# Performance work log

Measured on AMD Instinct MI355X. Metric: run time of the kernel, lower is better.

Reference implementation:

```python
import jax, jax.numpy as jnp
import numpy as np
from jax import lax

K = 4
H = 1024
IN = 512
OUT = 8192
T = 128
B = 32


def setup_inputs() -> dict:
    key = jax.random.key(0)
    ks = jax.random.split(key, 5)
    return {
        "X": jax.random.normal(ks[0], (T, B, IN), dtype=jnp.float32),
        "Wxh_w": jax.random.normal(ks[1], (H, IN), dtype=jnp.float32) * 0.02,
        "Wxh_b": jax.random.normal(ks[2], (H,), dtype=jnp.float32) * 0.02,
        "Whh_w": jax.random.normal(ks[3], (H, (K - 1) * H), dtype=jnp.float32) * 0.02,
        "Wmo_w": jax.random.normal(ks[4], (OUT, K * H), dtype=jnp.float32) * 0.02,
    }


def reference(X, Wxh_w, Wxh_b, Whh_w, Wmo_w):
    batch = X.shape[1]
    # history stack hs: [K-1, B, H], hs[0] = oldest, hs[-1] = newest
    hs0 = jnp.zeros((K - 1, batch, H), dtype=X.dtype)

    def step(hs, x_t):
        # concat reversed(h_prevs): newest block first -> [B, (K-1)*H]
        h_cat = hs[::-1].transpose(1, 0, 2).reshape(batch, (K - 1) * H)
        h_t = jax.nn.selu(x_t @ Wxh_w.T + Wxh_b + h_cat @ Whh_w.T)  # [B, H]
        h_out = jnp.concatenate([h_t, h_cat], axis=1)  # [B, K*H]
        out_t = h_out @ Wmo_w.T  # [B, OUT]
        new_hs = jnp.concatenate([hs[1:], h_t[None]], axis=0)
        # truncated BPTT: detach the (new) oldest hidden
        new_hs = new_hs.at[0].set(lax.stop_gradient(new_hs[0]))
        return new_hs, out_t

    _, outs = lax.scan(step, hs0, X)
    return outs  # [T, B, OUT]
```

## Files before the change

kernel.cpp:

```cpp
#include <hip/hip_runtime.h>
#include <hip/hip_bf16.h>

#define T_STEPS 128
#define BATCH   32
#define IN_DIM  512
#define H_DIM   1024
#define OUT_DIM 8192
#define KH      3072
#define NWG     128
#define SLOT_E  32768
#define NSLOT   131

typedef __attribute__((ext_vector_type(8))) short short8;
typedef __attribute__((ext_vector_type(4))) float f32x4;

__device__ __forceinline__ unsigned short bf16_rne(float f) {
  unsigned u = __float_as_uint(f);
  unsigned r = (u + 0x7FFFu + ((u >> 16) & 1u)) >> 16;
  return (unsigned short)r;
}

__device__ __forceinline__ void gload_lds16(const void* g, void* l) {
  __builtin_amdgcn_global_load_lds(
      (const __attribute__((address_space(1))) void*)g,
      (__attribute__((address_space(3))) void*)l, 16, 0, 0);
}

__global__ __launch_bounds__(256) void convert_kernel(
    const float* __restrict__ src, unsigned short* __restrict__ dst, int n4) {
  int i = blockIdx.x * blockDim.x + threadIdx.x;
  const int stride = gridDim.x * blockDim.x;
  for (; i < n4; i += stride) {
    float4 v = ((const float4*)src)[i];
    ushort4 o;
    o.x = bf16_rne(v.x); o.y = bf16_rne(v.y);
    o.z = bf16_rne(v.z); o.w = bf16_rne(v.w);
    ((ushort4*)dst)[i] = o;
  }
}

__global__ __launch_bounds__(256) void pre_kernel(
    const float* __restrict__ X, const float* __restrict__ Wxh,
    const float* __restrict__ bias, float* __restrict__ preT) {
  __shared__ float xs[32][260];
  const int tid = threadIdx.x;
  const int t  = blockIdx.x >> 4;
  const int jb = blockIdx.x & 15;
  const int b  = tid & 31;
  const int jg = tid >> 5;
  float acc[8];
  #pragma unroll
  for (int i = 0; i < 8; ++i) acc[i] = 0.f;

  for (int kc = 0; kc < 2; ++kc) {
    __syncthreads();
    #pragma unroll
    for (int v = tid; v < 2048; v += 256) {
      int br = v >> 6, i4 = v & 63;
      float4 x4 = *(const float4*)(X + (size_t)t*(BATCH*IN_DIM) + (size_t)br*IN_DIM + kc*256 + i4*4);
      *(float4*)&xs[br][i4*4] = x4;
    }
    __syncthreads();
    for (int i = 0; i < 256; i += 4) {
      const int k = kc*256 + i;
      float4 xv = *(const float4*)&xs[b][i];
      #pragma unroll
      for (int jj = 0; jj < 8; ++jj) {
        const int j = jb*64 + jg + jj*8;
        float4 w4 = *(const float4*)(Wxh + (size_t)j*IN_DIM + k);
        acc[jj] += xv.x*w4.x + xv.y*w4.y + xv.z*w4.z + xv.w*w4.w;
      }
    }
  }
  #pragma unroll
  for (int jj = 0; jj < 8; ++jj) {
    const int j = jb*64 + jg + jj*8;
    preT[(size_t)t*(H_DIM*BATCH) + (size_t)j*BATCH + b] = acc[jj] + bias[j];
  }
}

template<int RN, int RD1, int RD2>
__device__ __forceinline__ void do_step(
    const int t, const int tid, const int wg, const int j0,
    const int lane, const int wv,
    const short8* __restrict__ wf, const short8* __restrict__ hi8,
    const short8* __restrict__ lo8, const float* __restrict__ preT,
    unsigned short* __restrict__ hHi, unsigned short* __restrict__ hLo,
    int* __restrict__ grp, int* __restrict__ rootcnt, int* __restrict__ rootrep,
    short8 (&Rh0)[3][4], short8 (&Rh1)[3][4],
    short8 (&Rl0)[3][4], short8 (&Rl1)[3][4],
    float (&red)[8][16][33],
    unsigned short (&hpk_hi)[32][8], unsigned short (&hpk_lo)[32][8]) {
  f32x4 a0h = {}, a0l = {}, a1h = {}, a1l = {};

  #pragma unroll
  for (int i = 0; i < 4; ++i) {
    const int ks = 32 + wv*4 + i;
    const short8 af = wf[ks*64 + lane];
    a0h = __builtin_amdgcn_mfma_f32_16x16x32_bf16(af, Rh0[RD1][i], a0h, 0, 0, 0);
    a1h = __builtin_amdgcn_mfma_f32_16x16x32_bf16(af, Rh1[RD1][i], a1h, 0, 0, 0);
    a0l = __builtin_amdgcn_mfma_f32_16x16x32_bf16(af, Rl0[RD1][i], a0l, 0, 0, 0);
    a1l = __builtin_amdgcn_mfma_f32_16x16x32_bf16(af, Rl1[RD1][i], a1l, 0, 0, 0);
  }
  #pragma unroll
  for (int i = 0; i < 4; ++i) {
    const int ks = 64 + wv*4 + i;
    const short8 af = wf[ks*64 + lane];
    a0h = __builtin_amdgcn_mfma_f32_16x16x32_bf16(af, Rh0[RD2][i], a0h, 0, 0, 0);
    a1h = __builtin_amdgcn_mfma_f32_16x16x32_bf16(af, Rh1[RD2][i], a1h, 0, 0, 0);
    a0l = __builtin_amdgcn_mfma_f32_16x16x32_bf16(af, Rl0[RD2][i], a0l, 0, 0, 0);
    a1l = __builtin_amdgcn_mfma_f32_16x16x32_bf16(af, Rl1[RD2][i], a1l, 0, 0, 0);
  }

  float upre = 0.f;
  if (tid < 256)
    upre = preT[(size_t)t*(H_DIM*BATCH) + (size_t)(j0 + (tid >> 5))*BATCH + (tid & 31)];

  if (t > 0) {
    if (tid == 0) {
      while (!__hip_atomic_load(&rootrep[(((t-1) << 3) + (wg & 7)) << 4],
                                __ATOMIC_RELAXED, __HIP_MEMORY_SCOPE_AGENT))
        __builtin_amdgcn_s_sleep(2);
    }
    __syncthreads();
    asm volatile("" ::: "memory");
  }

  {
    const size_t sb = (size_t)(128 - t) * 4096;
    #pragma unroll
    for (int i = 0; i < 4; ++i) {
      const int ks = wv*4 + i;
      const size_t bidx = sb + (size_t)ks*128 + (size_t)(lane >> 4)*32 + (lane & 15);
      Rh0[RN][i] = hi8[bidx];
      Rh1[RN][i] = hi8[bidx + 16];
      Rl0[RN][i] = lo8[bidx];
      Rl1[RN][i] = lo8[bidx + 16];
    }
  }
  #pragma unroll
  for (int i = 0; i < 4; ++i) {
    const int ks = wv*4 + i;
    const short8 af = wf[ks*64 + lane];
    a0h = __builtin_amdgcn_mfma_f32_16x16x32_bf16(af, Rh0[RN][i], a0h, 0, 0, 0);
    a1h = __builtin_amdgcn_mfma_f32_16x16x32_bf16(af, Rh1[RN][i], a1h, 0, 0, 0);
    a0l = __builtin_amdgcn_mfma_f32_16x16x32_bf16(af, Rl0[RN][i], a0l, 0, 0, 0);
    a1l = __builtin_amdgcn_mfma_f32_16x16x32_bf16(af, Rl1[RN][i], a1l, 0, 0, 0);
  }

  const f32x4 s0 = a0h + a0l;
  const f32x4 s1 = a1h + a1l;
  const int rr = (lane >> 4) * 4, cc = lane & 15;
  #pragma unroll
  for (int q = 0; q < 4; ++q) {
    red[wv][rr + q][cc]      = s0[q];
    red[wv][rr + q][16 + cc] = s1[q];
  }
  __syncthreads();

  if (tid < 256) {
    const int jj = tid >> 5, b = tid & 31;
    float u = upre;
    #pragma unroll
    for (int w = 0; w < 8; ++w)
      u += red[w][jj][b] + red[w][jj + 8][b];
    const float h = u > 0.f ? 1.0507009873554805f*u
                            : (1.0507009873554805f*1.6732632423543772f)*expm1f(u);
    const unsigned short hh = bf16_rne(h);
    hpk_hi[b][jj] = hh;
    hpk_lo[b][jj] = bf16_rne(h - __uint_as_float((unsigned)hh << 16));
  }
  __syncthreads();

  if (tid < 32) {
    const int b = tid;
    const size_t base = (size_t)(127 - t)*SLOT_E + (size_t)(j0 >> 3)*256 + (size_t)b*8;
    const unsigned long long h0 = *(const unsigned long long*)&hpk_hi[b][0];
    const unsigned long long h1 = *(const unsigned long long*)&hpk_hi[b][4];
    const unsigned long long l0 = *(const unsigned long long*)&hpk_lo[b][0];
    const unsigned long long l1 = *(const unsigned long long*)&hpk_lo[b][4];
    __hip_atomic_store((unsigned long long*)(hHi + base),     h0, __ATOMIC_RELAXED, __HIP_MEMORY_SCOPE_AGENT);
    __hip_atomic_store((unsigned long long*)(hHi + base) + 1, h1, __ATOMIC_RELAXED, __HIP_MEMORY_SCOPE_AGENT);
    __hip_atomic_store((unsigned long long*)(hLo + base),     l0, __ATOMIC_RELAXED, __HIP_MEMORY_SCOPE_AGENT);
    __hip_atomic_store((unsigned long long*)(hLo + base) + 1, l1, __ATOMIC_RELAXED, __HIP_MEMORY_SCOPE_AGENT);
    if (t < T_STEPS - 1) {
      asm volatile("s_waitcnt vmcnt(0)" ::: "memory");
      if (tid == 0) {
        const int g = wg >> 3;
        if (__hip_atomic_fetch_add(&grp[((t << 4) + g) << 4], 1, __ATOMIC_RELAXED, __HIP_MEMORY_SCOPE_AGENT) == 7) {
          if (__hip_atomic_fetch_add(&rootcnt[t << 4], 1, __ATOMIC_RELAXED, __HIP_MEMORY_SCOPE_AGENT) == 15) {
            #pragma unroll
            for (int r = 0; r < 8; ++r)
              __hip_atomic_store(&rootrep[((t << 3) + r) << 4], 1,
                                 __ATOMIC_RELAXED, __HIP_MEMORY_SCOPE_AGENT);
          }
        }
      }
    }
  }
}

__global__ __launch_bounds__(512, 2) void recur_kernel(
    const float* __restrict__ Whh, const float* __restrict__ preT,
    unsigned short* __restrict__ hHi, unsigned short* __restrict__ hLo,
    int* __restrict__ grp, int* __restrict__ rootcnt, int* __restrict__ rootrep) {
  __shared__ __align__(16) unsigned short w_lds[96*64*8];
  __shared__ float red[8][16][33];
  __shared__ __align__(16) unsigned short hpk_hi[32][8];
  __shared__ __align__(16) unsigned short hpk_lo[32][8];
  const int tid  = threadIdx.x;
  const int wg   = blockIdx.x;
  const int j0   = wg * 8;
  const int lane = tid & 63;
  const int wv   = tid >> 6;

  for (int s = tid; s < 6144; s += 512) {
    const int ks = s >> 6, l = s & 63;
    const int r = l & 15;
    const int j = j0 + (r & 7);
    const int part = r >> 3;
    const int kb = ks*32 + (l >> 4)*8;
    const float* wp = Whh + (size_t)j*KH + kb;
    unsigned short tmp[8];
    #pragma unroll
    for (int i = 0; i < 8; ++i) {
      const float f = wp[i];
      unsigned short v = bf16_rne(f);
      if (part) v = bf16_rne(f - __uint_as_float((unsigned)v << 16));
      tmp[i] = v;
    }
    *(short8*)&w_lds[s*8] = *(short8*)tmp;
  }
  __syncthreads();

  const short8* wf  = (const short8*)w_lds;
  const short8* hi8 = (const short8*)hHi;
  const short8* lo8 = (const short8*)hLo;

  short8 Rh0[3][4], Rh1[3][4], Rl0[3][4], Rl1[3][4];
  const short8 z8 = {};
  #pragma unroll
  for (int r = 1; r < 3; ++r)
    #pragma unroll
    for (int i = 0; i < 4; ++i) {
      Rh0[r][i] = z8; Rh1[r][i] = z8; Rl0[r][i] = z8; Rl1[r][i] = z8;
    }

  for (int t3 = 0; t3 < 126; t3 += 3) {
    do_step<0,2,1>(t3,   tid, wg, j0, lane, wv, wf, hi8, lo8, preT, hHi, hLo,
                   grp, rootcnt, rootrep, Rh0, Rh1, Rl0, Rl1, red, hpk_hi, hpk_lo);
    do_step<1,0,2>(t3+1, tid, wg, j0, lane, wv, wf, hi8, lo8, preT, hHi, hLo,
                   grp, rootcnt, rootrep, Rh0, Rh1, Rl0, Rl1, red, hpk_hi, hpk_lo);
    do_step<2,1,0>(t3+2, tid, wg, j0, lane, wv, wf, hi8, lo8, preT, hHi, hLo,
                   grp, rootcnt, rootrep, Rh0, Rh1, Rl0, Rl1, red, hpk_hi, hpk_lo);
  }
  do_step<0,2,1>(126, tid, wg, j0, lane, wv, wf, hi8, lo8, preT, hHi, hLo,
                 grp, rootcnt, rootrep, Rh0, Rh1, Rl0, Rl1, red, hpk_hi, hpk_lo);
  do_step<1,0,2>(127, tid, wg, j0, lane, wv, wf, hi8, lo8, preT, hHi, hLo,
                 grp, rootcnt, rootrep, Rh0, Rh1, Rl0, Rl1, red, hpk_hi, hpk_lo);
}

__global__ __launch_bounds__(512, 2) void gemm256_kernel(
    const unsigned short* __restrict__ Ah, const unsigned short* __restrict__ Bm,
    float* __restrict__ C) {
  extern __shared__ char smem[];
  const int tid = threadIdx.x;
  const int wg = blockIdx.x;
  const int x = wg & 7;
  const int c = wg >> 3;
  const int mb = c & 15;
  const int nb = x*4 + (c >> 4);
  const int lane = tid & 63;
  const int wv = tid >> 6;
  const int wm = wv >> 2;
  const int wn = wv & 3;
  const int lrow = lane & 15, lhalf = lane >> 4;
  const int srow = tid & 127;
  const int ss0 = tid >> 7;
  int tA[2], bA[2];
  #pragma unroll
  for (int h = 0; h < 2; ++h) {
    const int m = mb*256 + h*128 + srow;
    tA[h] = m >> 5; bA[h] = m & 31;
  }

#define STAGE_A(HALF, BUF, KT) do {                                            \
    _Pragma("unroll")                                                          \
    for (int u = 0; u < 2; ++u) {                                              \
      const int s_ = u*4 + ss0;                                                \
      gload_lds16(Ah + (size_t)(127 - tA[HALF])*SLOT_E                         \
                     + (size_t)((KT)*8 + s_)*256 + bA[HALF]*8,                 \
                  smem + (BUF)*65536 + (HALF)*16384 + u*8192 + tid*16);        \
    } } while (0)

#define STAGE_B(HALF, BUF, KT) do {                                            \
    _Pragma("unroll")                                                          \
    for (int u = 0; u < 2; ++u) {                                              \
      const int s_ = u*4 + ss0;                                                \
      gload_lds16(Bm + (size_t)(nb*256 + (HALF)*128 + srow)*4096               \
                     + (size_t)(KT)*64 + s_*8,                                 \
                  smem + (BUF)*65536 + 32768 + (HALF)*16384 + u*8192 + tid*16);\
    } } while (0)

  short8 aF[4][2], bF[2][2];
  f32x4 acc[8][4] = {};

#define PHASE(BUF, MH, NH, RDA, RDB, STAGE_STMT, DO_VM) do {                   \
    if (RDA) {                                                                 \
      _Pragma("unroll")                                                        \
      for (int mi = 0; mi < 4; ++mi)                                           \
        _Pragma("unroll")                                                      \
        for (int kk = 0; kk < 2; ++kk)                                         \
          aF[mi][kk] = *(const short8*)(smem + (BUF)*65536 + wm*16384          \
              + (kk*4 + lhalf)*2048 + ((MH)*64 + mi*16 + lrow)*16);            \
    }                                                                          \
    if (RDB) {                                                                 \
      _Pragma("unroll")                                                        \
      for (int ni = 0; ni < 2; ++ni)                                           \
        _Pragma("unroll")                                                      \
        for (int kk = 0; kk < 2; ++kk)                                         \
          bF[ni][kk] = *(const short8*)(smem + (BUF)*65536 + 32768             \
              + (wn >> 1)*16384 + (kk*4 + lhalf)*2048                          \
              + ((wn & 1)*64 + (NH)*32 + ni*16 + lrow)*16);                    \
    }                                                                          \
    STAGE_STMT;                                                                \
    __builtin_amdgcn_s_barrier();                                              \
    __builtin_amdgcn_s_setprio(1);                                             \
    _Pragma("unroll")                                                          \
    for (int mi = 0; mi < 4; ++mi)                                             \
      _Pragma("unroll")                                                        \
      for (int ni = 0; ni < 2; ++ni) {                                         \
        acc[(MH)*4+mi][(NH)*2+ni] = __builtin_amdgcn_mfma_f32_16x16x32_bf16(   \
            aF[mi][0], bF[ni][0], acc[(MH)*4+mi][(NH)*2+ni], 0, 0, 0);         \
        acc[(MH)*4+mi][(NH)*2+ni] = __builtin_amdgcn_mfma_f32_16x16x32_bf16(   \
            aF[mi][1], bF[ni][1], acc[(MH)*4+mi][(NH)*2+ni], 0, 0, 0);         \
      }                                                                        \
    __builtin_amdgcn_s_setprio(0);                                             \
    if (DO_VM) asm volatile("s_waitcnt vmcnt(2)" ::: "memory");                \
    __builtin_amdgcn_s_barrier();                                              \
  } while (0)

  STAGE_A(0, 0, 0);
  STAGE_B(0, 0, 0);
  STAGE_B(1, 0, 0);
  STAGE_A(1, 0, 0);
  STAGE_A(0, 1, 1);
  asm volatile("s_waitcnt vmcnt(2)" ::: "memory");
  __builtin_amdgcn_s_barrier();

  for (int j = 0; j < 32; ++j) {
    const int k1 = 2*j + 1;
    const int k2 = (2*j + 2 < 64) ? 2*j + 2 : 63;
    const int k3 = (2*j + 3 < 64) ? 2*j + 3 : 63;
    PHASE(0, 0, 0, 1, 1, STAGE_B(0, 1, k1), 0);
    PHASE(0, 0, 1, 0, 1, STAGE_B(1, 1, k1), 0);
    PHASE(0, 1, 1, 1, 0, STAGE_A(1, 1, k1), 0);
    PHASE(0, 1, 0, 0, 1, STAGE_A(0, 0, k2), 1);
    PHASE(1, 0, 0, 1, 1, STAGE_B(0, 0, k2), 0);
    PHASE(1, 0, 1, 0, 1, STAGE_B(1, 0, k2), 0);
    PHASE(1, 1, 1, 1, 0, STAGE_A(1, 0, k2), 0);
    PHASE(1, 1, 0, 0, 1, STAGE_A(0, 1, k3), 1);
  }
#undef PHASE
#undef STAGE_A
#undef STAGE_B

  const int orow0 = mb*256 + wm*128 + lhalf*4;
  const int ocol0 = nb*256 + wn*64 + lrow;
  #pragma unroll
  for (int m_ = 0; m_ < 8; ++m_)
    #pragma unroll
    for (int n_ = 0; n_ < 4; ++n_)
      #pragma unroll
      for (int q = 0; q < 4; ++q)
        __builtin_nontemporal_store(acc[m_][n_][q],
            &C[(size_t)(orow0 + m_*16 + q)*OUT_DIM + ocol0 + n_*16]);
}

extern "C" void kernel_launch(void* const* d_in, const int* in_sizes, int n_in,
                              void* d_out, int out_size, void* d_ws, size_t ws_size,
                              hipStream_t stream) {
  (void)in_sizes; (void)n_in; (void)out_size; (void)ws_size;
  const float* X   = (const float*)d_in[0];
  const float* Wxh = (const float*)d_in[1];
  const float* Wxb = (const float*)d_in[2];
  const float* Whh = (const float*)d_in[3];
  const float* Wmo = (const float*)d_in[4];
  float* out = (float*)d_out;
  char* ws = (char*)d_ws;

  const size_t OFF_PRET = 0;
  const size_t OFF_HHI  = OFF_PRET + (size_t)T_STEPS*H_DIM*BATCH*4;
  const size_t OFF_HLO  = OFF_HHI + (size_t)NSLOT*SLOT_E*2;
  const size_t OFF_GRP  = OFF_HLO + (size_t)NSLOT*SLOT_E*2;
  const size_t OFF_RCNT = OFF_GRP + (size_t)T_STEPS*16*64;
  const size_t OFF_RREP = OFF_RCNT + (size_t)T_STEPS*64;
  const size_t OFF_W16  = OFF_RREP + (size_t)T_STEPS*8*64;

  float* preT = (float*)(ws + OFF_PRET);
  unsigned short* hHi = (unsigned short*)(ws + OFF_HHI);
  unsigned short* hLo = (unsigned short*)(ws + OFF_HLO);
  int* grp     = (int*)(ws + OFF_GRP);
  int* rootcnt = (int*)(ws + OFF_RCNT);
  int* rootrep = (int*)(ws + OFF_RREP);
  unsigned short* Wmo16 = (unsigned short*)(ws + OFF_W16);

  (void)hipFuncSetAttribute(reinterpret_cast<const void*>(gemm256_kernel),
                            hipFuncAttributeMaxDynamicSharedMemorySize, 131072);

  hipMemsetAsync(hHi + (size_t)128*SLOT_E, 0, (size_t)3*SLOT_E*2, stream);
  hipMemsetAsync(hLo + (size_t)128*SLOT_E, 0, (size_t)3*SLOT_E*2, stream);
  hipMemsetAsync(grp, 0, (size_t)T_STEPS*16*64 + (size_t)T_STEPS*64
                        + (size_t)T_STEPS*8*64, stream);

  convert_kernel<<<2048, 256, 0, stream>>>(Wmo, Wmo16, (int)((size_t)OUT_DIM*4096/4));
  pre_kernel<<<2048, 256, 0, stream>>>(X, Wxh, Wxb, preT);
  recur_kernel<<<NWG, 512, 0, stream>>>(Whh, preT, hHi, hLo, grp, rootcnt, rootrep);
  gemm256_kernel<<<512, 512, 131072, stream>>>(hHi, Wmo16, out);
}
```

Measured before the change: 1.060 ms.

## Fuse recurrence and output GEMM into one persistent kernel with ticketed tiles

```diff
diff --git a/kernel.cpp b/kernel.cpp
--- a/kernel.cpp
+++ b/kernel.cpp
@@ -10,6 +10,7 @@
 #define NWG     128
 #define SLOT_E  32768
 #define NSLOT   131
+#define NTILE   512
 
 typedef __attribute__((ext_vector_type(8))) short short8;
 typedef __attribute__((ext_vector_type(4))) float f32x4;
@@ -89,8 +90,8 @@
     int* __restrict__ grp, int* __restrict__ rootcnt, int* __restrict__ rootrep,
     short8 (&Rh0)[3][4], short8 (&Rh1)[3][4],
     short8 (&Rl0)[3][4], short8 (&Rl1)[3][4],
-    float (&red)[8][16][33],
-    unsigned short (&hpk_hi)[32][8], unsigned short (&hpk_lo)[32][8]) {
+    float (*red)[16][33],
+    unsigned short (*hpk_hi)[8], unsigned short (*hpk_lo)[8]) {
   f32x4 a0h = {}, a0l = {}, a1h = {}, a1l = {};
 
   #pragma unroll
@@ -183,93 +184,24 @@
     __hip_atomic_store((unsigned long long*)(hHi + base) + 1, h1, __ATOMIC_RELAXED, __HIP_MEMORY_SCOPE_AGENT);
     __hip_atomic_store((unsigned long long*)(hLo + base),     l0, __ATOMIC_RELAXED, __HIP_MEMORY_SCOPE_AGENT);
     __hip_atomic_store((unsigned long long*)(hLo + base) + 1, l1, __ATOMIC_RELAXED, __HIP_MEMORY_SCOPE_AGENT);
-    if (t < T_STEPS - 1) {
-      asm volatile("s_waitcnt vmcnt(0)" ::: "memory");
-      if (tid == 0) {
-        const int g = wg >> 3;
-        if (__hip_atomic_fetch_add(&grp[((t << 4) + g) << 4], 1, __ATOMIC_RELAXED, __HIP_MEMORY_SCOPE_AGENT) == 7) {
-          if (__hip_atomic_fetch_add(&rootcnt[t << 4], 1, __ATOMIC_RELAXED, __HIP_MEMORY_SCOPE_AGENT) == 15) {
-            #pragma unroll
-            for (int r = 0; r < 8; ++r)
-              __hip_atomic_store(&rootrep[((t << 3) + r) << 4], 1,
-                                 __ATOMIC_RELAXED, __HIP_MEMORY_SCOPE_AGENT);
-          }
+    asm volatile("s_waitcnt vmcnt(0)" ::: "memory");
+    if (tid == 0) {
+      const int g = wg >> 3;
+      if (__hip_atomic_fetch_add(&grp[((t << 4) + g) << 4], 1, __ATOMIC_RELAXED, __HIP_MEMORY_SCOPE_AGENT) == 7) {
+        if (__hip_atomic_fetch_add(&rootcnt[t << 4], 1, __ATOMIC_RELAXED, __HIP_MEMORY_SCOPE_AGENT) == 15) {
+          #pragma unroll
+          for (int r = 0; r < 8; ++r)
+            __hip_atomic_store(&rootrep[((t << 3) + r) << 4], 1,
+                               __ATOMIC_RELAXED, __HIP_MEMORY_SCOPE_AGENT);
         }
       }
     }
   }
 }
 
-__global__ __launch_bounds__(512, 2) void recur_kernel(
-    const float* __restrict__ Whh, const float* __restrict__ preT,
-    unsigned short* __restrict__ hHi, unsigned short* __restrict__ hLo,
-    int* __restrict__ grp, int* __restrict__ rootcnt, int* __restrict__ rootrep) {
-  __shared__ __align__(16) unsigned short w_lds[96*64*8];
-  __shared__ float red[8][16][33];
-  __shared__ __align__(16) unsigned short hpk_hi[32][8];
-  __shared__ __align__(16) unsigned short hpk_lo[32][8];
-  const int tid  = threadIdx.x;
-  const int wg   = blockIdx.x;
-  const int j0   = wg * 8;
-  const int lane = tid & 63;
-  const int wv   = tid >> 6;
-
-  for (int s = tid; s < 6144; s += 512) {
-    const int ks = s >> 6, l = s & 63;
-    const int r = l & 15;
-    const int j = j0 + (r & 7);
-    const int part = r >> 3;
-    const int kb = ks*32 + (l >> 4)*8;
-    const float* wp = Whh + (size_t)j*KH + kb;
-    unsigned short tmp[8];
-    #pragma unroll
-    for (int i = 0; i < 8; ++i) {
-      const float f = wp[i];
-      unsigned short v = bf16_rne(f);
-      if (part) v = bf16_rne(f - __uint_as_float((unsigned)v << 16));
-      tmp[i] = v;
-    }
-    *(short8*)&w_lds[s*8] = *(short8*)tmp;
-  }
-  __syncthreads();
-
-  const short8* wf  = (const short8*)w_lds;
-  const short8* hi8 = (const short8*)hHi;
-  const short8* lo8 = (const short8*)hLo;
-
-  short8 Rh0[3][4], Rh1[3][4], Rl0[3][4], Rl1[3][4];
-  const short8 z8 = {};
-  #pragma unroll
-  for (int r = 1; r < 3; ++r)
-    #pragma unroll
-    for (int i = 0; i < 4; ++i) {
-      Rh0[r][i] = z8; Rh1[r][i] = z8; Rl0[r][i] = z8; Rl1[r][i] = z8;
-    }
-
-  for (int t3 = 0; t3 < 126; t3 += 3) {
-    do_step<0,2,1>(t3,   tid, wg, j0, lane, wv, wf, hi8, lo8, preT, hHi, hLo,
-                   grp, rootcnt, rootrep, Rh0, Rh1, Rl0, Rl1, red, hpk_hi, hpk_lo);
-    do_step<1,0,2>(t3+1, tid, wg, j0, lane, wv, wf, hi8, lo8, preT, hHi, hLo,
-                   grp, rootcnt, rootrep, Rh0, Rh1, Rl0, Rl1, red, hpk_hi, hpk_lo);
-    do_step<2,1,0>(t3+2, tid, wg, j0, lane, wv, wf, hi8, lo8, preT, hHi, hLo,
-                   grp, rootcnt, rootrep, Rh0, Rh1, Rl0, Rl1, red, hpk_hi, hpk_lo);
-  }
-  do_step<0,2,1>(126, tid, wg, j0, lane, wv, wf, hi8, lo8, preT, hHi, hLo,
-                 grp, rootcnt, rootrep, Rh0, Rh1, Rl0, Rl1, red, hpk_hi, hpk_lo);
-  do_step<1,0,2>(127, tid, wg, j0, lane, wv, wf, hi8, lo8, preT, hHi, hLo,
-                 grp, rootcnt, rootrep, Rh0, Rh1, Rl0, Rl1, red, hpk_hi, hpk_lo);
-}
-
-__global__ __launch_bounds__(512, 2) void gemm256_kernel(
+__device__ void gemm_tile256(
     const unsigned short* __restrict__ Ah, const unsigned short* __restrict__ Bm,
-    float* __restrict__ C) {
-  extern __shared__ char smem[];
-  const int tid = threadIdx.x;
-  const int wg = blockIdx.x;
-  const int x = wg & 7;
-  const int c = wg >> 3;
-  const int mb = c & 15;
-  const int nb = x*4 + (c >> 4);
+    float* __restrict__ C, char* smem, const int tid, const int mb, const int nb) {
   const int lane = tid & 63;
   const int wv = tid >> 6;
   const int wm = wv >> 2;
@@ -377,6 +309,93 @@
             &C[(size_t)(orow0 + m_*16 + q)*OUT_DIM + ocol0 + n_*16]);
 }
 
+__global__ __launch_bounds__(512, 2) void fused_kernel(
+    const float* __restrict__ Whh, const float* __restrict__ preT,
+    unsigned short* __restrict__ hHi, unsigned short* __restrict__ hLo,
+    int* __restrict__ grp, int* __restrict__ rootcnt, int* __restrict__ rootrep,
+    int* __restrict__ ticket, const unsigned short* __restrict__ Wmo16,
+    float* __restrict__ C) {
+  extern __shared__ char smem[];
+  __shared__ int tk_ls;
+  const int tid = threadIdx.x;
+  const int wg  = blockIdx.x;
+
+  if (wg < NWG) {
+    unsigned short* w_lds = (unsigned short*)smem;
+    float (*red)[16][33] = (float (*)[16][33])(smem + 98304);
+    unsigned short (*hpk_hi)[8] = (unsigned short (*)[8])(smem + 115200);
+    unsigned short (*hpk_lo)[8] = (unsigned short (*)[8])(smem + 115712);
+    const int j0   = wg * 8;
+    const int lane = tid & 63;
+    const int wv   = tid >> 6;
+
+    for (int s = tid; s < 6144; s += 512) {
+      const int ks = s >> 6, l = s & 63;
+      const int r = l & 15;
+      const int j = j0 + (r & 7);
+      const int part = r >> 3;
+      const int kb = ks*32 + (l >> 4)*8;
+      const float* wp = Whh + (size_t)j*KH + kb;
+      unsigned short tmp[8];
+      #pragma unroll
+      for (int i = 0; i < 8; ++i) {
+        const float f = wp[i];
+        unsigned short v = bf16_rne(f);
+        if (part) v = bf16_rne(f - __uint_as_float((unsigned)v << 16));
+        tmp[i] = v;
+      }
+      *(short8*)&w_lds[s*8] = *(short8*)tmp;
+    }
+    __syncthreads();
+
+    const short8* wf  = (const short8*)w_lds;
+    const short8* hi8 = (const short8*)hHi;
+    const short8* lo8 = (const short8*)hLo;
+
+    short8 Rh0[3][4], Rh1[3][4], Rl0[3][4], Rl1[3][4];
+    const short8 z8 = {};
+    #pragma unroll
+    for (int r = 1; r < 3; ++r)
+      #pragma unroll
+      for (int i = 0; i < 4; ++i) {
+        Rh0[r][i] = z8; Rh1[r][i] = z8; Rl0[r][i] = z8; Rl1[r][i] = z8;
+      }
+
+    for (int t3 = 0; t3 < 126; t3 += 3) {
+      do_step<0,2,1>(t3,   tid, wg, j0, lane, wv, wf, hi8, lo8, preT, hHi, hLo,
+                     grp, rootcnt, rootrep, Rh0, Rh1, Rl0, Rl1, red, hpk_hi, hpk_lo);
+      do_step<1,0,2>(t3+1, tid, wg, j0, lane, wv, wf, hi8, lo8, preT, hHi, hLo,
+                     grp, rootcnt, rootrep, Rh0, Rh1, Rl0, Rl1, red, hpk_hi, hpk_lo);
+      do_step<2,1,0>(t3+2, tid, wg, j0, lane, wv, wf, hi8, lo8, preT, hHi, hLo,
+                     grp, rootcnt, rootrep, Rh0, Rh1, Rl0, Rl1, red, hpk_hi, hpk_lo);
+    }
+    do_step<0,2,1>(126, tid, wg, j0, lane, wv, wf, hi8, lo8, preT, hHi, hLo,
+                   grp, rootcnt, rootrep, Rh0, Rh1, Rl0, Rl1, red, hpk_hi, hpk_lo);
+    do_step<1,0,2>(127, tid, wg, j0, lane, wv, wf, hi8, lo8, preT, hHi, hLo,
+                   grp, rootcnt, rootrep, Rh0, Rh1, Rl0, Rl1, red, hpk_hi, hpk_lo);
+    __syncthreads();
+  }
+
+  for (;;) {
+    if (tid == 0)
+      tk_ls = __hip_atomic_fetch_add(ticket, 1, __ATOMIC_RELAXED, __HIP_MEMORY_SCOPE_AGENT);
+    __syncthreads();
+    const int tk = tk_ls;
+    __syncthreads();
+    if (tk >= NTILE) return;
+    const int mb = tk >> 5, nb = tk & 31;
+    if (tid == 0) {
+      while (!__hip_atomic_load(&rootrep[(((8*mb + 7) << 3) + (wg & 7)) << 4],
+                                __ATOMIC_RELAXED, __HIP_MEMORY_SCOPE_AGENT))
+        __builtin_amdgcn_s_sleep(2);
+    }
+    __syncthreads();
+    asm volatile("" ::: "memory");
+    gemm_tile256(hHi, Wmo16, C, smem, tid, mb, nb);
+    __syncthreads();
+  }
+}
+
 extern "C" void kernel_launch(void* const* d_in, const int* in_sizes, int n_in,
                               void* d_out, int out_size, void* d_ws, size_t ws_size,
                               hipStream_t stream) {
@@ -395,7 +414,8 @@
   const size_t OFF_GRP  = OFF_HLO + (size_t)NSLOT*SLOT_E*2;
   const size_t OFF_RCNT = OFF_GRP + (size_t)T_STEPS*16*64;
   const size_t OFF_RREP = OFF_RCNT + (size_t)T_STEPS*64;
-  const size_t OFF_W16  = OFF_RREP + (size_t)T_STEPS*8*64;
+  const size_t OFF_TKT  = OFF_RREP + (size_t)T_STEPS*8*64;
+  const size_t OFF_W16  = OFF_TKT + 64;
 
   float* preT = (float*)(ws + OFF_PRET);
   unsigned short* hHi = (unsigned short*)(ws + OFF_HHI);
@@ -403,18 +423,19 @@
   int* grp     = (int*)(ws + OFF_GRP);
   int* rootcnt = (int*)(ws + OFF_RCNT);
   int* rootrep = (int*)(ws + OFF_RREP);
+  int* ticket  = (int*)(ws + OFF_TKT);
   unsigned short* Wmo16 = (unsigned short*)(ws + OFF_W16);
 
-  (void)hipFuncSetAttribute(reinterpret_cast<const void*>(gemm256_kernel),
+  (void)hipFuncSetAttribute(reinterpret_cast<const void*>(fused_kernel),
                             hipFuncAttributeMaxDynamicSharedMemorySize, 131072);
 
   hipMemsetAsync(hHi + (size_t)128*SLOT_E, 0, (size_t)3*SLOT_E*2, stream);
   hipMemsetAsync(hLo + (size_t)128*SLOT_E, 0, (size_t)3*SLOT_E*2, stream);
   hipMemsetAsync(grp, 0, (size_t)T_STEPS*16*64 + (size_t)T_STEPS*64
-                        + (size_t)T_STEPS*8*64, stream);
+                        + (size_t)T_STEPS*8*64 + 64, stream);
 
   convert_kernel<<<2048, 256, 0, stream>>>(Wmo, Wmo16, (int)((size_t)OUT_DIM*4096/4));
   pre_kernel<<<2048, 256, 0, stream>>>(X, Wxh, Wxb, preT);
-  recur_kernel<<<NWG, 512, 0, stream>>>(Whh, preT, hHi, hLo, grp, rootcnt, rootrep);
-  gemm256_kernel<<<512, 512, 131072, stream>>>(hHi, Wmo16, out);
-}
+  fused_kernel<<<256, 512, 131072, stream>>>(Whh, preT, hHi, hLo, grp, rootcnt,
+                                             rootrep, ticket, Wmo16, out);
+}
```

Result: slower. 1.720 ms (+62.3%).
